# Performance work log

Hardware: AMD Instinct MI355X
Metric: run time of the kernel (lower is better)

## Reference

```python
import jax, jax.numpy as jnp
import numpy as np

T, B, FEAT = 256, 512, 8
HID = 256
IN_DIM = 4  # QCNN output dim


def _linear_params(key, out_dim, in_dim, scale=0.1):
    kw, kb = jax.random.split(key)
    W = jax.random.normal(kw, (out_dim, in_dim), dtype=jnp.float32) * scale
    b = jax.random.normal(kb, (out_dim,), dtype=jnp.float32) * scale
    return W, b


def setup_inputs() -> dict:
    key = jax.random.key(0)
    ks = jax.random.split(key, 12)
    inputs = jax.random.normal(ks[0], (T, B, FEAT), dtype=jnp.float32)
    # QCNN feature extractor linears (torch Linear: W is [out, in])
    fm_w, fm_b = _linear_params(ks[1], 16, FEAT)
    c1_w, c1_b = _linear_params(ks[2], 16, 16)
    p1_w, p1_b = _linear_params(ks[3], 12, 16)
    c2_w, c2_b = _linear_params(ks[4], 8, 12)
    p2_w, p2_b = _linear_params(ks[5], 4, 8)
    c3_w, c3_b = _linear_params(ks[6], 4, 4)
    # LSTM gate linears: (IN_DIM + HID) -> HID
    f_w, f_b = _linear_params(ks[7], HID, IN_DIM + HID)
    i_w, i_b = _linear_params(ks[8], HID, IN_DIM + HID)
    u_w, u_b = _linear_params(ks[9], HID, IN_DIM + HID)
    o_w, o_b = _linear_params(ks[10], HID, IN_DIM + HID)
    # tagger head: HID -> 1
    head_w, head_b = _linear_params(ks[11], 1, HID)
    return dict(inputs=inputs, fm_w=fm_w, fm_b=fm_b, c1_w=c1_w, c1_b=c1_b,
                p1_w=p1_w, p1_b=p1_b, c2_w=c2_w, c2_b=c2_b, p2_w=p2_w, p2_b=p2_b,
                c3_w=c3_w, c3_b=c3_b, f_w=f_w, f_b=f_b, i_w=i_w, i_b=i_b,
                u_w=u_w, u_b=u_b, o_w=o_w, o_b=o_b, head_w=head_w, head_b=head_b)


def _lin(x, W, b):
    return x @ W.T + b


def reference(inputs, fm_w, fm_b, c1_w, c1_b, p1_w, p1_b, c2_w, c2_b,
              p2_w, p2_b, c3_w, c3_b, f_w, f_b, i_w, i_b, u_w, u_b,
              o_w, o_b, head_w, head_b):
    seq_len, batch, _ = inputs.shape
    # QCNN feature extractor has no cross-timestep dependency -> apply to all steps at once
    x = jnp.tanh(_lin(inputs, fm_w, fm_b))
    x = jnp.tanh(_lin(x, c1_w, c1_b))
    x = jnp.tanh(_lin(x, p1_w, p1_b))
    x = jnp.tanh(_lin(x, c2_w, c2_b))
    x = jnp.tanh(_lin(x, p2_w, p2_b))
    feats = jnp.tanh(_lin(x, c3_w, c3_b))  # [T, B, 4]

    h0 = jnp.zeros((batch, HID), dtype=inputs.dtype)
    c0 = jnp.zeros((batch, HID), dtype=inputs.dtype)

    def step(carry, xt):
        hx, cx = carry
        combined = jnp.concatenate([xt, hx], axis=1)  # [B, 4+HID]
        f = jax.nn.sigmoid(_lin(combined, f_w, f_b))
        i = jax.nn.sigmoid(_lin(combined, i_w, i_b))
        g = jnp.tanh(_lin(combined, u_w, u_b))
        o = jax.nn.sigmoid(_lin(combined, o_w, o_b))
        cx = f * cx + i * g
        hx = o * jnp.tanh(cx)
        return (hx, cx), hx

    (_, _), lstm_out = jax.lax.scan(step, (h0, c0), feats)  # [T, B, HID]
    out = _lin(lstm_out, head_w, head_b)  # [T, B, 1]
    return out
```

## Files before the change

kernel.cpp:

```cpp
#include <hip/hip_runtime.h>
#include <hip/hip_bf16.h>
#include <hip/hip_fp16.h>
#include <stdint.h>

#define T_STEPS 256
#define BATCH 512

typedef _Float16 f16x8 __attribute__((ext_vector_type(8)));
typedef _Float16 h2_t  __attribute__((ext_vector_type(2)));
typedef float    f32x4 __attribute__((ext_vector_type(4)));

__device__ __forceinline__ float fdot2(uint32_t w, uint32_t c, float acc) {
#if __has_builtin(__builtin_amdgcn_fdot2)
    h2_t a, b;
    __builtin_memcpy(&a, &w, 4);
    __builtin_memcpy(&b, &c, 4);
    return __builtin_amdgcn_fdot2(a, b, acc, false);
#else
    union { uint32_t u; _Float16 h[2]; } A, B;
    A.u = w; B.u = c;
    return acc + (float)A.h[0]*(float)B.h[0] + (float)A.h[1]*(float)B.h[1];
#endif
}

__device__ __forceinline__ float sigmoidf_(float x) {
    return 1.f / (1.f + __expf(-x));
}
__device__ __forceinline__ float tanhf_(float x) {
    float ax = fabsf(x);
    float e = __expf(-2.f * ax);
    float r = (1.f - e) / (1.f + e);
    return copysignf(r, x);
}

#define MFMA_AG(c, aa, bb) \
    asm volatile("v_mfma_f32_16x16x32_f16 %0, %1, %2, %0" : "+v"(c) : "v"(aa), "a"(bb))
#define MFMA_VG(c, aa, bb) \
    asm volatile("v_mfma_f32_16x16x32_f16 %0, %1, %2, %0" : "+v"(c) : "v"(aa), "v"(bb))

__global__ void concat_qw(const float* __restrict__ fm_w, const float* __restrict__ fm_b,
                          const float* __restrict__ c1_w, const float* __restrict__ c1_b,
                          const float* __restrict__ p1_w, const float* __restrict__ p1_b,
                          const float* __restrict__ c2_w, const float* __restrict__ c2_b,
                          const float* __restrict__ p2_w, const float* __restrict__ p2_b,
                          const float* __restrict__ c3_w, const float* __restrict__ c3_b,
                          float* __restrict__ qw) {
    for (int k = threadIdx.x; k < 780; k += 256) {
        float v;
        if      (k < 128) v = fm_w[k];
        else if (k < 144) v = fm_b[k-128];
        else if (k < 400) v = c1_w[k-144];
        else if (k < 416) v = c1_b[k-400];
        else if (k < 608) v = p1_w[k-416];
        else if (k < 620) v = p1_b[k-608];
        else if (k < 716) v = c2_w[k-620];
        else if (k < 724) v = c2_b[k-716];
        else if (k < 756) v = p2_w[k-724];
        else if (k < 760) v = p2_b[k-756];
        else if (k < 776) v = c3_w[k-760];
        else              v = c3_b[k-776];
        qw[k] = v;
    }
}

__global__ void pack_bfrag(const float* __restrict__ f_w, const float* __restrict__ i_w,
                           const float* __restrict__ u_w, const float* __restrict__ o_w,
                           uint4* __restrict__ bfragsG) {
    int idx = blockIdx.x * 256 + threadIdx.x;
    int l = idx & 63, q = (idx >> 6) & 7, n = idx >> 9;
    int col = n * 16 + (l & 15);
    int g = col >> 8, j = col & 255;
    const float* W = (g == 0) ? f_w : (g == 1) ? i_w : (g == 2) ? u_w : o_w;
    union { uint4 u; _Float16 h[8]; } P;
#pragma unroll
    for (int e = 0; e < 8; ++e) {
        int k = q * 32 + ((l >> 4) * 8) + e;
        P.h[e] = (_Float16)W[j * 260 + 4 + k];
    }
    bfragsG[idx] = P.u;
}

__global__ void pack_xw(const float* __restrict__ f_w, const float* __restrict__ i_w,
                        const float* __restrict__ u_w, const float* __restrict__ o_w,
                        _Float16* __restrict__ xwG) {
    int t = blockIdx.x * 256 + threadIdx.x;
    int g = t >> 10, k = (t >> 8) & 3, j = t & 255;
    const float* W = (g == 0) ? f_w : (g == 1) ? i_w : (g == 2) ? u_w : o_w;
    xwG[t] = (_Float16)W[j * 260 + k];
}

__global__ void qcnn_kernel(const float* __restrict__ in, const float* __restrict__ qw,
                            _Float16* __restrict__ feats) {
    int r = blockIdx.x * 256 + threadIdx.x;
    const float* x = in + (size_t)r * 8;
    float v0[8];
#pragma unroll
    for (int i = 0; i < 8; ++i) v0[i] = x[i];
    float v1[16];
#pragma unroll
    for (int o = 0; o < 16; ++o) {
        float s = qw[128 + o];
#pragma unroll
        for (int i = 0; i < 8; ++i) s += qw[o*8 + i] * v0[i];
        v1[o] = tanhf_(s);
    }
    float v2[16];
#pragma unroll
    for (int o = 0; o < 16; ++o) {
        float s = qw[400 + o];
#pragma unroll
        for (int i = 0; i < 16; ++i) s += qw[144 + o*16 + i] * v1[i];
        v2[o] = tanhf_(s);
    }
    float v3[12];
#pragma unroll
    for (int o = 0; o < 12; ++o) {
        float s = qw[608 + o];
#pragma unroll
        for (int i = 0; i < 16; ++i) s += qw[416 + o*16 + i] * v2[i];
        v3[o] = tanhf_(s);
    }
    float v4[8];
#pragma unroll
    for (int o = 0; o < 8; ++o) {
        float s = qw[716 + o];
#pragma unroll
        for (int i = 0; i < 12; ++i) s += qw[620 + o*12 + i] * v3[i];
        v4[o] = tanhf_(s);
    }
    float v5[4];
#pragma unroll
    for (int o = 0; o < 4; ++o) {
        float s = qw[756 + o];
#pragma unroll
        for (int i = 0; i < 8; ++i) s += qw[724 + o*8 + i] * v4[i];
        v5[o] = tanhf_(s);
    }
    union { uint32_t u[2]; _Float16 h[4]; } P;
#pragma unroll
    for (int o = 0; o < 4; ++o) {
        float s = qw[776 + o];
#pragma unroll
        for (int i = 0; i < 4; ++i) s += qw[760 + o*4 + i] * v5[i];
        P.h[o] = (_Float16)tanhf_(s);
    }
    *reinterpret_cast<uint2*>(feats + (size_t)r * 4) = make_uint2(P.u[0], P.u[1]);
}

__global__ __launch_bounds__(256, 1)
void lstm_kernel(const uint4* __restrict__ bfragsG, const _Float16* __restrict__ xwG,
                 const _Float16* __restrict__ feats,
                 const float* __restrict__ f_b, const float* __restrict__ i_b,
                 const float* __restrict__ u_b, const float* __restrict__ o_b,
                 const float* __restrict__ head_w, const float* __restrict__ head_bp,
                 float* __restrict__ out) {
    __shared__ uint4     bldsQ67[2][64][64];
    __shared__ uint4     bldsQ5o[16][64];
    __shared__ float     stripL[4][4][64][2];
    __shared__ __align__(16) _Float16 combL[2][2][256];
    __shared__ float     redL[2][2][4];

    const int tid = threadIdx.x;
    const int w   = tid >> 6;
    const int l   = tid & 63;
    const int s0  = blockIdx.x * 2;
    const int j   = w * 64 + l;

    for (int i = tid; i < 8192; i += 256) {
        int n = i >> 7, qq = (i >> 6) & 1, ll = i & 63;
        bldsQ67[qq][n][ll] = bfragsG[(n * 8 + 6 + qq) * 64 + ll];
    }
    for (int i = tid; i < 1024; i += 256) {
        int nn = i >> 6, ll = i & 63;
        bldsQ5o[nn][ll] = bfragsG[((48 + nn) * 8 + 5) * 64 + ll];
    }
    reinterpret_cast<uint32_t*>(&combL[0][0][0])[tid] = 0u;

    f16x8 Breg[16][6];
#pragma unroll
    for (int m = 0; m < 16; ++m) {
        const int n = (m >> 2) * 16 + w * 4 + (m & 3);
#pragma unroll
        for (int q = 0; q < 6; ++q) {
            if (m >= 12 && q == 5) continue;
            Breg[m][q] = *reinterpret_cast<const f16x8*>(bfragsG + (n * 8 + q) * 64 + l);
            asm volatile("" : "+a"(Breg[m][q]));
        }
    }

    float bias_[4] = { f_b[j], i_b[j], u_b[j], o_b[j] };
    const float hwj = head_w[j];
    const float hb  = head_bp[0];
    uint32_t xw01[4], xw23[4];
#pragma unroll
    for (int g = 0; g < 4; ++g) {
        union { uint32_t u; _Float16 h[2]; } P;
        P.h[0] = xwG[g*1024 +       j]; P.h[1] = xwG[g*1024 + 256 + j];
        xw01[g] = P.u;
        P.h[0] = xwG[g*1024 + 512 + j]; P.h[1] = xwG[g*1024 + 768 + j];
        xw23[g] = P.u;
    }
    uint2 xr0 = *reinterpret_cast<const uint2*>(feats + ((size_t)0 * BATCH + s0    ) * 4);
    uint2 xr1 = *reinterpret_cast<const uint2*>(feats + ((size_t)0 * BATCH + s0 + 1) * 4);

    __syncthreads();

    float cs0 = 0.f, cs1 = 0.f;

#pragma unroll 1
    for (int t = 0; t < T_STEPS; ++t) {
        uint2 xn0 = xr0, xn1 = xr1;
        if (t + 1 < T_STEPS) {
            xn0 = *reinterpret_cast<const uint2*>(feats + ((size_t)(t+1) * BATCH + s0    ) * 4);
            xn1 = *reinterpret_cast<const uint2*>(feats + ((size_t)(t+1) * BATCH + s0 + 1) * 4);
        }

        const _Float16* abase = &combL[t & 1][l & 1][(l >> 4) * 8];
        f16x8 A_[8];
#pragma unroll
        for (int q = 0; q < 8; ++q)
            A_[q] = *reinterpret_cast<const f16x8*>(abase + q * 32);

#pragma unroll
        for (int b = 0; b < 4; ++b) {
            f16x8 t6[4], t7[4], t5[4];
#pragma unroll
            for (int d = 0; d < 4; ++d) {
                const int n = b * 16 + w * 4 + d;
                t6[d] = *reinterpret_cast<const f16x8*>(&bldsQ67[0][n][l]);
                t7[d] = *reinterpret_cast<const f16x8*>(&bldsQ67[1][n][l]);
            }
            if (b == 3) {
#pragma unroll
                for (int d = 0; d < 4; ++d)
                    t5[d] = *reinterpret_cast<const f16x8*>(&bldsQ5o[w * 4 + d][l]);
            }

            f32x4 c0 = {0.f,0.f,0.f,0.f}, c1 = {0.f,0.f,0.f,0.f};
            f32x4 c2 = {0.f,0.f,0.f,0.f}, c3 = {0.f,0.f,0.f,0.f};
            asm volatile("s_nop 1" : "+v"(c0), "+v"(c1), "+v"(c2), "+v"(c3));

            MFMA_VG(c0, A_[6], t6[0]); MFMA_VG(c1, A_[6], t6[1]);
            MFMA_VG(c2, A_[6], t6[2]); MFMA_VG(c3, A_[6], t6[3]);
            MFMA_VG(c0, A_[7], t7[0]); MFMA_VG(c1, A_[7], t7[1]);
            MFMA_VG(c2, A_[7], t7[2]); MFMA_VG(c3, A_[7], t7[3]);
            if (b == 3) {
                MFMA_VG(c0, A_[5], t5[0]); MFMA_VG(c1, A_[5], t5[1]);
                MFMA_VG(c2, A_[5], t5[2]); MFMA_VG(c3, A_[5], t5[3]);
            }
#pragma unroll
            for (int q = 0; q < 5; ++q) {
                MFMA_AG(c0, A_[q], Breg[4*b+0][q]); MFMA_AG(c1, A_[q], Breg[4*b+1][q]);
                MFMA_AG(c2, A_[q], Breg[4*b+2][q]); MFMA_AG(c3, A_[q], Breg[4*b+3][q]);
            }
            if (b < 3) {
                MFMA_AG(c0, A_[5], Breg[4*b+0][5]); MFMA_AG(c1, A_[5], Breg[4*b+1][5]);
                MFMA_AG(c2, A_[5], Breg[4*b+2][5]); MFMA_AG(c3, A_[5], Breg[4*b+3][5]);
            }

            asm volatile("s_nop 7\n\ts_nop 7" : "+v"(c0), "+v"(c1), "+v"(c2), "+v"(c3));

            if (l < 16) {
                *reinterpret_cast<float2*>(&stripL[w][b][0*16 + l][0]) = make_float2(c0[0], c0[1]);
                *reinterpret_cast<float2*>(&stripL[w][b][1*16 + l][0]) = make_float2(c1[0], c1[1]);
                *reinterpret_cast<float2*>(&stripL[w][b][2*16 + l][0]) = make_float2(c2[0], c2[1]);
                *reinterpret_cast<float2*>(&stripL[w][b][3*16 + l][0]) = make_float2(c3[0], c3[1]);
            }
        }

        asm volatile("s_waitcnt lgkmcnt(0)" ::: "memory");
        __builtin_amdgcn_wave_barrier();

        float pre0[4], pre1[4];
#pragma unroll
        for (int g = 0; g < 4; ++g) {
            float2 gv = *reinterpret_cast<const float2*>(&stripL[w][g][l][0]);
            pre0[g] = fdot2(xw01[g], xr0.x, fdot2(xw23[g], xr0.y, gv.x + bias_[g]));
            pre1[g] = fdot2(xw01[g], xr1.x, fdot2(xw23[g], xr1.y, gv.y + bias_[g]));
        }
        const float fg0 = sigmoidf_(pre0[0]), fg1 = sigmoidf_(pre1[0]);
        const float ig0 = sigmoidf_(pre0[1]), ig1 = sigmoidf_(pre1[1]);
        const float ug0 = tanhf_(pre0[2]),    ug1 = tanhf_(pre1[2]);
        const float og0 = sigmoidf_(pre0[3]), og1 = sigmoidf_(pre1[3]);
        cs0 = fg0 * cs0 + ig0 * ug0;
        cs1 = fg1 * cs1 + ig1 * ug1;
        const float h0 = og0 * tanhf_(cs0);
        const float h1 = og1 * tanhf_(cs1);

        _Float16* nb = &combL[(t + 1) & 1][0][0];
        nb[j]       = (_Float16)h0;
        nb[256 + j] = (_Float16)h1;

        float p0 = h0 * hwj, p1 = h1 * hwj;
#pragma unroll
        for (int off = 32; off; off >>= 1) {
            p0 += __shfl_down(p0, off);
            p1 += __shfl_down(p1, off);
        }
        if (l == 0) { redL[t & 1][0][w] = p0; redL[t & 1][1][w] = p1; }

        xr0 = xn0; xr1 = xn1;
        __syncthreads();

        if (tid < 2)
            out[(size_t)t * BATCH + s0 + tid] =
                (redL[t & 1][tid][0] + redL[t & 1][tid][1]) +
                (redL[t & 1][tid][2] + redL[t & 1][tid][3]) + hb;
    }
}

extern "C" void kernel_launch(void* const* d_in, const int* in_sizes, int n_in,
                              void* d_out, int out_size, void* d_ws, size_t ws_size,
                              hipStream_t stream) {
    const float* inputs = (const float*)d_in[0];
    const float* fm_w = (const float*)d_in[1];  const float* fm_b = (const float*)d_in[2];
    const float* c1_w = (const float*)d_in[3];  const float* c1_b = (const float*)d_in[4];
    const float* p1_w = (const float*)d_in[5];  const float* p1_b = (const float*)d_in[6];
    const float* c2_w = (const float*)d_in[7];  const float* c2_b = (const float*)d_in[8];
    const float* p2_w = (const float*)d_in[9];  const float* p2_b = (const float*)d_in[10];
    const float* c3_w = (const float*)d_in[11]; const float* c3_b = (const float*)d_in[12];
    const float* f_w  = (const float*)d_in[13]; const float* f_b  = (const float*)d_in[14];
    const float* i_w  = (const float*)d_in[15]; const float* i_b  = (const float*)d_in[16];
    const float* u_w  = (const float*)d_in[17]; const float* u_b  = (const float*)d_in[18];
    const float* o_w  = (const float*)d_in[19]; const float* o_b  = (const float*)d_in[20];
    const float* head_w = (const float*)d_in[21];
    const float* head_b = (const float*)d_in[22];

    uint4*     bfragsG = (uint4*)d_ws;
    _Float16*  xwG     = (_Float16*)((char*)d_ws + 524288);
    _Float16*  feats   = (_Float16*)((char*)d_ws + 532480);
    float*     qw      = (float*)((char*)d_ws + 1581056);

    hipLaunchKernelGGL(concat_qw, dim3(1), dim3(256), 0, stream,
                       fm_w, fm_b, c1_w, c1_b, p1_w, p1_b, c2_w, c2_b,
                       p2_w, p2_b, c3_w, c3_b, qw);
    hipLaunchKernelGGL(pack_bfrag, dim3(128), dim3(256), 0, stream,
                       f_w, i_w, u_w, o_w, bfragsG);
    hipLaunchKernelGGL(pack_xw, dim3(16), dim3(256), 0, stream,
                       f_w, i_w, u_w, o_w, xwG);
    hipLaunchKernelGGL(qcnn_kernel, dim3(512), dim3(256), 0, stream,
                       inputs, qw, feats);
    hipLaunchKernelGGL(lstm_kernel, dim3(256), dim3(256), 0, stream,
                       bfragsG, xwG, feats,
                       f_b, i_b, u_b, o_b, head_w, head_b, (float*)d_out);
}
```

Baseline: 705.9 us.

## Select gate results in registers and restructure B fragment placement across AGPR/LDS/global

Gate preactivations are now picked from MFMA accumulators with a per-lane select instead of going through an LDS strip buffer and wave barrier. The hidden-unit mapping per lane changes to match the accumulator layout. B fragments are redistributed: K-slices 0-3 stay in AGPRs, 4-5 move to LDS, and slices 6-7 are read from global memory (through cache) every step. The aim is to cut LDS round trips and register pressure, at the cost of per-step global loads on the serial critical path.

```diff
diff --git a/kernel.cpp b/kernel.cpp
--- a/kernel.cpp
+++ b/kernel.cpp
@@ -33,10 +33,14 @@
     return copysignf(r, x);
 }
 
+__device__ __forceinline__ float sel4(int d, float a, float b, float c, float e) {
+    float lo = (d & 1) ? b : a;
+    float hi = (d & 1) ? e : c;
+    return (d & 2) ? hi : lo;
+}
+
 #define MFMA_AG(c, aa, bb) \
     asm volatile("v_mfma_f32_16x16x32_f16 %0, %1, %2, %0" : "+v"(c) : "v"(aa), "a"(bb))
-#define MFMA_VG(c, aa, bb) \
-    asm volatile("v_mfma_f32_16x16x32_f16 %0, %1, %2, %0" : "+v"(c) : "v"(aa), "v"(bb))
 
 __global__ void concat_qw(const float* __restrict__ fm_w, const float* __restrict__ fm_b,
                           const float* __restrict__ c1_w, const float* __restrict__ c1_b,
@@ -154,52 +158,51 @@
                  const float* __restrict__ u_b, const float* __restrict__ o_b,
                  const float* __restrict__ head_w, const float* __restrict__ head_bp,
                  float* __restrict__ out) {
-    __shared__ uint4     bldsQ67[2][64][64];
-    __shared__ uint4     bldsQ5o[16][64];
-    __shared__ float     stripL[4][4][64][2];
-    __shared__ __align__(16) _Float16 combL[2][2][256];
-    __shared__ float     redL[2][2][4];
+    __shared__ uint4     blds45[2][64][64];
+    __shared__ uint4     blds6o[16][64];
+    __shared__ __align__(16) _Float16 comb[2][2][256];
+    __shared__ float     redL[2][4][2];
 
     const int tid = threadIdx.x;
     const int w   = tid >> 6;
     const int l   = tid & 63;
+    const int d_  = l >> 4;
+    const int jl  = (w * 4 + d_) * 16 + (l & 15);
     const int s0  = blockIdx.x * 2;
-    const int j   = w * 64 + l;
-
-    for (int i = tid; i < 8192; i += 256) {
-        int n = i >> 7, qq = (i >> 6) & 1, ll = i & 63;
-        bldsQ67[qq][n][ll] = bfragsG[(n * 8 + 6 + qq) * 64 + ll];
-    }
-    for (int i = tid; i < 1024; i += 256) {
-        int nn = i >> 6, ll = i & 63;
-        bldsQ5o[nn][ll] = bfragsG[((48 + nn) * 8 + 5) * 64 + ll];
-    }
-    reinterpret_cast<uint32_t*>(&combL[0][0][0])[tid] = 0u;
-
-    f16x8 Breg[16][6];
+
+    for (int idx = tid; idx < 8192; idx += 256) {
+        int n = idx >> 7, qq = (idx >> 6) & 1, ll = idx & 63;
+        blds45[qq][n][ll] = bfragsG[(n * 8 + 4 + qq) * 64 + ll];
+    }
+    for (int idx = tid; idx < 1024; idx += 256) {
+        int nn = idx >> 6, ll = idx & 63;
+        blds6o[nn][ll] = bfragsG[((48 + nn) * 8 + 6) * 64 + ll];
+    }
+    reinterpret_cast<uint32_t*>(&comb[0][0][0])[tid] = 0u;
+
+    f16x8 Br[16][4];
 #pragma unroll
     for (int m = 0; m < 16; ++m) {
         const int n = (m >> 2) * 16 + w * 4 + (m & 3);
 #pragma unroll
-        for (int q = 0; q < 6; ++q) {
-            if (m >= 12 && q == 5) continue;
-            Breg[m][q] = *reinterpret_cast<const f16x8*>(bfragsG + (n * 8 + q) * 64 + l);
-            asm volatile("" : "+a"(Breg[m][q]));
-        }
-    }
-
-    float bias_[4] = { f_b[j], i_b[j], u_b[j], o_b[j] };
-    const float hwj = head_w[j];
-    const float hb  = head_bp[0];
-    uint32_t xw01[4], xw23[4];
+        for (int q = 0; q < 4; ++q) {
+            Br[m][q] = *reinterpret_cast<const f16x8*>(bfragsG + (n * 8 + q) * 64 + l);
+            asm volatile("" : "+a"(Br[m][q]));
+        }
+    }
+
+    float bias_[4] = { f_b[jl], i_b[jl], u_b[jl], o_b[jl] };
+    uint32_t xwp0[4], xwp1[4];
 #pragma unroll
     for (int g = 0; g < 4; ++g) {
         union { uint32_t u; _Float16 h[2]; } P;
-        P.h[0] = xwG[g*1024 +       j]; P.h[1] = xwG[g*1024 + 256 + j];
-        xw01[g] = P.u;
-        P.h[0] = xwG[g*1024 + 512 + j]; P.h[1] = xwG[g*1024 + 768 + j];
-        xw23[g] = P.u;
-    }
+        P.h[0] = xwG[g*1024 +       jl]; P.h[1] = xwG[g*1024 + 256 + jl];
+        xwp0[g] = P.u;
+        P.h[0] = xwG[g*1024 + 512 + jl]; P.h[1] = xwG[g*1024 + 768 + jl];
+        xwp1[g] = P.u;
+    }
+    const float hwj = head_w[jl];
+    const float hb  = head_bp[0];
     uint2 xr0 = *reinterpret_cast<const uint2*>(feats + ((size_t)0 * BATCH + s0    ) * 4);
     uint2 xr1 = *reinterpret_cast<const uint2*>(feats + ((size_t)0 * BATCH + s0 + 1) * 4);
 
@@ -209,74 +212,74 @@
 
 #pragma unroll 1
     for (int t = 0; t < T_STEPS; ++t) {
+        const int cur = t & 1;
         uint2 xn0 = xr0, xn1 = xr1;
         if (t + 1 < T_STEPS) {
             xn0 = *reinterpret_cast<const uint2*>(feats + ((size_t)(t+1) * BATCH + s0    ) * 4);
             xn1 = *reinterpret_cast<const uint2*>(feats + ((size_t)(t+1) * BATCH + s0 + 1) * 4);
         }
 
-        const _Float16* abase = &combL[t & 1][l & 1][(l >> 4) * 8];
+        const _Float16* ab = &comb[cur][l & 1][(l >> 4) * 8];
         f16x8 A_[8];
 #pragma unroll
         for (int q = 0; q < 8; ++q)
-            A_[q] = *reinterpret_cast<const f16x8*>(abase + q * 32);
-
-#pragma unroll
-        for (int b = 0; b < 4; ++b) {
-            f16x8 t6[4], t7[4], t5[4];
+            A_[q] = *reinterpret_cast<const f16x8*>(ab + q * 32);
+
+        float gv0[4], gv1[4];
+
+#pragma unroll
+        for (int g = 0; g < 4; ++g) {
+            f16x8 s6[4], s7[4];
 #pragma unroll
             for (int d = 0; d < 4; ++d) {
-                const int n = b * 16 + w * 4 + d;
-                t6[d] = *reinterpret_cast<const f16x8*>(&bldsQ67[0][n][l]);
-                t7[d] = *reinterpret_cast<const f16x8*>(&bldsQ67[1][n][l]);
+                const int n = g * 16 + w * 4 + d;
+                if (g < 3) s6[d] = *reinterpret_cast<const f16x8*>(bfragsG + (n * 8 + 6) * 64 + l);
+                else       s6[d] = *reinterpret_cast<const f16x8*>(&blds6o[w * 4 + d][l]);
+                s7[d] = *reinterpret_cast<const f16x8*>(bfragsG + (n * 8 + 7) * 64 + l);
             }
-            if (b == 3) {
-#pragma unroll
-                for (int d = 0; d < 4; ++d)
-                    t5[d] = *reinterpret_cast<const f16x8*>(&bldsQ5o[w * 4 + d][l]);
+            f16x8 b4[4], b5[4];
+#pragma unroll
+            for (int d = 0; d < 4; ++d) {
+                const int n = g * 16 + w * 4 + d;
+                b4[d] = *reinterpret_cast<const f16x8*>(&blds45[0][n][l]);
+                b5[d] = *reinterpret_cast<const f16x8*>(&blds45[1][n][l]);
             }
 
             f32x4 c0 = {0.f,0.f,0.f,0.f}, c1 = {0.f,0.f,0.f,0.f};
             f32x4 c2 = {0.f,0.f,0.f,0.f}, c3 = {0.f,0.f,0.f,0.f};
-            asm volatile("s_nop 1" : "+v"(c0), "+v"(c1), "+v"(c2), "+v"(c3));
-
-            MFMA_VG(c0, A_[6], t6[0]); MFMA_VG(c1, A_[6], t6[1]);
-            MFMA_VG(c2, A_[6], t6[2]); MFMA_VG(c3, A_[6], t6[3]);
-            MFMA_VG(c0, A_[7], t7[0]); MFMA_VG(c1, A_[7], t7[1]);
-            MFMA_VG(c2, A_[7], t7[2]); MFMA_VG(c3, A_[7], t7[3]);
-            if (b == 3) {
-                MFMA_VG(c0, A_[5], t5[0]); MFMA_VG(c1, A_[5], t5[1]);
-                MFMA_VG(c2, A_[5], t5[2]); MFMA_VG(c3, A_[5], t5[3]);
+            asm volatile("s_nop 0" : "+v"(c0), "+v"(c1), "+v"(c2), "+v"(c3));
+
+#pragma unroll
+            for (int q = 0; q < 4; ++q) {
+                MFMA_AG(c0, A_[q], Br[4*g+0][q]); MFMA_AG(c1, A_[q], Br[4*g+1][q]);
+                MFMA_AG(c2, A_[q], Br[4*g+2][q]); MFMA_AG(c3, A_[q], Br[4*g+3][q]);
             }
-#pragma unroll
-            for (int q = 0; q < 5; ++q) {
-                MFMA_AG(c0, A_[q], Breg[4*b+0][q]); MFMA_AG(c1, A_[q], Breg[4*b+1][q]);
-                MFMA_AG(c2, A_[q], Breg[4*b+2][q]); MFMA_AG(c3, A_[q], Breg[4*b+3][q]);
-            }
-            if (b < 3) {
-                MFMA_AG(c0, A_[5], Breg[4*b+0][5]); MFMA_AG(c1, A_[5], Breg[4*b+1][5]);
-                MFMA_AG(c2, A_[5], Breg[4*b+2][5]); MFMA_AG(c3, A_[5], Breg[4*b+3][5]);
-            }
-
-            asm volatile("s_nop 7\n\ts_nop 7" : "+v"(c0), "+v"(c1), "+v"(c2), "+v"(c3));
-
-            if (l < 16) {
-                *reinterpret_cast<float2*>(&stripL[w][b][0*16 + l][0]) = make_float2(c0[0], c0[1]);
-                *reinterpret_cast<float2*>(&stripL[w][b][1*16 + l][0]) = make_float2(c1[0], c1[1]);
-                *reinterpret_cast<float2*>(&stripL[w][b][2*16 + l][0]) = make_float2(c2[0], c2[1]);
-                *reinterpret_cast<float2*>(&stripL[w][b][3*16 + l][0]) = make_float2(c3[0], c3[1]);
-            }
-        }
-
-        asm volatile("s_waitcnt lgkmcnt(0)" ::: "memory");
-        __builtin_amdgcn_wave_barrier();
+            c0 = __builtin_amdgcn_mfma_f32_16x16x32_f16(A_[4], b4[0], c0, 0, 0, 0);
+            c1 = __builtin_amdgcn_mfma_f32_16x16x32_f16(A_[4], b4[1], c1, 0, 0, 0);
+            c2 = __builtin_amdgcn_mfma_f32_16x16x32_f16(A_[4], b4[2], c2, 0, 0, 0);
+            c3 = __builtin_amdgcn_mfma_f32_16x16x32_f16(A_[4], b4[3], c3, 0, 0, 0);
+            c0 = __builtin_amdgcn_mfma_f32_16x16x32_f16(A_[5], b5[0], c0, 0, 0, 0);
+            c1 = __builtin_amdgcn_mfma_f32_16x16x32_f16(A_[5], b5[1], c1, 0, 0, 0);
+            c2 = __builtin_amdgcn_mfma_f32_16x16x32_f16(A_[5], b5[2], c2, 0, 0, 0);
+            c3 = __builtin_amdgcn_mfma_f32_16x16x32_f16(A_[5], b5[3], c3, 0, 0, 0);
+            c0 = __builtin_amdgcn_mfma_f32_16x16x32_f16(A_[6], s6[0], c0, 0, 0, 0);
+            c1 = __builtin_amdgcn_mfma_f32_16x16x32_f16(A_[6], s6[1], c1, 0, 0, 0);
+            c2 = __builtin_amdgcn_mfma_f32_16x16x32_f16(A_[6], s6[2], c2, 0, 0, 0);
+            c3 = __builtin_amdgcn_mfma_f32_16x16x32_f16(A_[6], s6[3], c3, 0, 0, 0);
+            c0 = __builtin_amdgcn_mfma_f32_16x16x32_f16(A_[7], s7[0], c0, 0, 0, 0);
+            c1 = __builtin_amdgcn_mfma_f32_16x16x32_f16(A_[7], s7[1], c1, 0, 0, 0);
+            c2 = __builtin_amdgcn_mfma_f32_16x16x32_f16(A_[7], s7[2], c2, 0, 0, 0);
+            c3 = __builtin_amdgcn_mfma_f32_16x16x32_f16(A_[7], s7[3], c3, 0, 0, 0);
+
+            gv0[g] = sel4(d_, c0[0], c1[0], c2[0], c3[0]);
+            gv1[g] = sel4(d_, c0[1], c1[1], c2[1], c3[1]);
+        }
 
         float pre0[4], pre1[4];
 #pragma unroll
         for (int g = 0; g < 4; ++g) {
-            float2 gv = *reinterpret_cast<const float2*>(&stripL[w][g][l][0]);
-            pre0[g] = fdot2(xw01[g], xr0.x, fdot2(xw23[g], xr0.y, gv.x + bias_[g]));
-            pre1[g] = fdot2(xw01[g], xr1.x, fdot2(xw23[g], xr1.y, gv.y + bias_[g]));
+            pre0[g] = fdot2(xwp0[g], xr0.x, fdot2(xwp1[g], xr0.y, gv0[g] + bias_[g]));
+            pre1[g] = fdot2(xwp0[g], xr1.x, fdot2(xwp1[g], xr1.y, gv1[g] + bias_[g]));
         }
         const float fg0 = sigmoidf_(pre0[0]), fg1 = sigmoidf_(pre1[0]);
         const float ig0 = sigmoidf_(pre0[1]), ig1 = sigmoidf_(pre1[1]);
@@ -287,25 +290,24 @@
         const float h0 = og0 * tanhf_(cs0);
         const float h1 = og1 * tanhf_(cs1);
 
-        _Float16* nb = &combL[(t + 1) & 1][0][0];
-        nb[j]       = (_Float16)h0;
-        nb[256 + j] = (_Float16)h1;
+        comb[cur ^ 1][0][jl] = (_Float16)h0;
+        comb[cur ^ 1][1][jl] = (_Float16)h1;
 
         float p0 = h0 * hwj, p1 = h1 * hwj;
 #pragma unroll
         for (int off = 32; off; off >>= 1) {
-            p0 += __shfl_down(p0, off);
-            p1 += __shfl_down(p1, off);
-        }
-        if (l == 0) { redL[t & 1][0][w] = p0; redL[t & 1][1][w] = p1; }
+            p0 += __shfl_xor(p0, off);
+            p1 += __shfl_xor(p1, off);
+        }
+        if (l == 0) { redL[cur][w][0] = p0; redL[cur][w][1] = p1; }
 
         xr0 = xn0; xr1 = xn1;
         __syncthreads();
 
         if (tid < 2)
             out[(size_t)t * BATCH + s0 + tid] =
-                (redL[t & 1][tid][0] + redL[t & 1][tid][1]) +
-                (redL[t & 1][tid][2] + redL[t & 1][tid][3]) + hb;
+                (redL[cur][0][tid] + redL[cur][1][tid]) +
+                (redL[cur][2][tid] + redL[cur][3][tid]) + hb;
     }
 }
 
```

After: 635.8 us (median of 2 runs). 9.9% less time.
